# Kernel optimization log

Hardware: AMD Instinct MI355X
Metric: run time of the kernel (lower is better)

## Reference

```python
import jax, jax.numpy as jnp
import numpy as np

B, SEG, MEM, D, E, H = 4, 1024, 1024, 128, 128, 8  # model_dim == embed_dim required by module
TOTAL = SEG + MEM


def sinusoid_pos(length, e):
    # Transformer-XL relative sinusoid table, then flipped so row 0 = largest distance
    p = jnp.arange(length, dtype=jnp.float32)[:, None]
    j = jnp.arange(e, dtype=jnp.float32)[None, :]
    ang = p / jnp.power(jnp.float32(10000.0), 2.0 * j / e)
    enc = jnp.where((jnp.arange(e) % 2 == 0)[None, :], jnp.sin(ang), jnp.cos(ang))
    return enc[::-1]


def circulant_shift(b, shift):
    # b: (B, H, S, W). Row i of the index matrix is the rolled arange shifted by (shift - i).
    W = b.shape[-1]
    S = b.shape[-2]
    idx = jnp.roll(jnp.arange(W), shift)[::-1]
    idx2 = jnp.concatenate([idx, idx])
    win = idx2[jnp.arange(S)[:, None] + jnp.arange(W)[None, :]][:, ::-1]  # (S, W)
    return jnp.take_along_axis(b, win[None, None, :, :], axis=3)


def setup_inputs() -> dict:
    key = jax.random.key(0)
    ks = jax.random.split(key, 11)
    w = 0.02  # small init for linear weights (Linear default-ish scale)
    return {
        "x": jax.random.normal(ks[0], (B, SEG, D), dtype=jnp.float32),
        "mem": jax.random.normal(ks[1], (B, MEM, D), dtype=jnp.float32),
        "att_mask": jnp.zeros((SEG, TOTAL), dtype=bool),  # unused by the module's forward
        "u1": jax.random.normal(ks[2], (H, 1, E), dtype=jnp.float32),
        "u2": jax.random.normal(ks[3], (H, 1, E), dtype=jnp.float32),
        "w_q": jax.random.normal(ks[4], (D, H * E), dtype=jnp.float32) * w,
        "w_kv": jax.random.normal(ks[5], (D, 2 * H * E), dtype=jnp.float32) * w,
        "w_r": jax.random.normal(ks[6], (D, H * E), dtype=jnp.float32) * w,
        "w_mlp": jax.random.normal(ks[7], (H * E, D), dtype=jnp.float32) * w,
        "ln_g": jnp.ones((D,), dtype=jnp.float32),
        "ln_b": jnp.zeros((D,), dtype=jnp.float32),
    }


def reference(x, mem, att_mask, u1, u2, w_q, w_kv, w_r, w_mlp, ln_g, ln_b):
    bsz, seg, d = x.shape
    h = jnp.concatenate((mem, x), axis=1)          # (B, total, D)
    total = h.shape[1]
    mem_len = total - seg

    # NB: the original uses .view without transpose -> plain row-major reshape
    q = (x @ w_q).reshape(bsz, -1, seg, d)          # (B, H, S, E)
    kv = (h @ w_kv).reshape(2 * bsz, -1, total, d)  # (2B, H, T, E)
    k, v = kv[:bsz], kv[bsz:]

    pos = sinusoid_pos(total, d)                    # buffer pos[-total:]
    r = (pos @ w_r).reshape(-1, total, d)           # (H, T, E)

    b = jnp.einsum('bhse,hte->bhst', q, r)
    b = circulant_shift(b, -seg + 1)

    qk = jnp.einsum('bhse,bhte->bhst', q, k)
    u1k = jnp.einsum('he,bhte->bht', u1[:, 0], k)[:, :, None, :]
    u2r = jnp.einsum('he,hte->ht', u2[:, 0], r)[None, :, None, :]

    score = qk + b + u1k + u2r                      # (B, H, S, T)
    tri = (jnp.arange(total)[None, :] - jnp.arange(seg)[:, None]) <= mem_len
    score = jnp.where(tri[None, None], score, 0.0) / jnp.sqrt(jnp.float32(d))
    score = jnp.where(score == 0.0, -jnp.inf, score)  # faithful zeros->-inf trick
    score = jax.nn.softmax(score, axis=-1)

    att = jnp.einsum('bhst,bhte->bhse', score, v).reshape(bsz, seg, -1)
    y = att @ w_mlp + x
    mu = jnp.mean(y, axis=-1, keepdims=True)
    var = jnp.mean((y - mu) ** 2, axis=-1, keepdims=True)
    return (y - mu) / jnp.sqrt(var + 1e-5) * ln_g + ln_b
```

## Files before the change

kernel.cpp:

```cpp
#include <hip/hip_runtime.h>
#include <hip/hip_bf16.h>
#include <stdint.h>

typedef __bf16 bf16;
typedef __attribute__((ext_vector_type(8))) __bf16 bf16x8;
typedef __attribute__((ext_vector_type(4))) __bf16 bf16x4;
typedef __attribute__((ext_vector_type(4))) float f32x4;

#define KSC 0.12764932952880681f

__device__ __forceinline__ f32x4 MFMA(bf16x8 a, bf16x8 b, f32x4 c) {
  return __builtin_amdgcn_mfma_f32_16x16x32_bf16(a, b, c, 0, 0, 0);
}

__device__ __forceinline__ void GLL16(const void* g, void* l) {
  __builtin_amdgcn_global_load_lds(
      (const __attribute__((address_space(1))) void*)g,
      (__attribute__((address_space(3))) void*)l, 16, 0, 0);
}

__device__ __forceinline__ bf16 tobf(float f) { return (bf16)f; }

__global__ __launch_bounds__(256) void k_prep(
    const float* __restrict__ x, const float* __restrict__ mm,
    const float* __restrict__ wq, const float* __restrict__ wkv,
    const float* __restrict__ wr, const float* __restrict__ wmlp,
    bf16* __restrict__ posb, bf16* __restrict__ wq_bt, bf16* __restrict__ wkv_bt,
    bf16* __restrict__ wr_bt, bf16* __restrict__ wmlp_bt,
    bf16* __restrict__ xb, bf16* __restrict__ memb)
{
  __shared__ float T[32][33];
  const int b = blockIdx.x;
  const int tid = threadIdx.x;
  if (b < 1024) {
    int id = b * 256 + tid;
    int t = id >> 7, j = id & 127;
    float p = (float)(2047 - t);
    float ang = p * exp2f(-(float)j * 0.20762050593046264f);
    float v = ((j & 1) == 0) ? __sinf(ang) : __cosf(ang);
    posb[id] = tobf(v);
    return;
  }
  if (b < 1664) {
    int tb = b - 1024;
    const float* src; bf16* dst; int R, C, r0, c0;
    if (tb < 128)      { src = wq;   dst = wq_bt;   R = 128;  C = 1024; r0 = (tb >> 5) * 32;        c0 = (tb & 31) * 32; }
    else if (tb < 384) { int t2 = tb - 128; src = wkv;  dst = wkv_bt;  R = 128;  C = 2048; r0 = (t2 >> 6) * 32; c0 = (t2 & 63) * 32; }
    else if (tb < 512) { int t2 = tb - 384; src = wr;   dst = wr_bt;   R = 128;  C = 1024; r0 = (t2 >> 5) * 32; c0 = (t2 & 31) * 32; }
    else               { int t2 = tb - 512; src = wmlp; dst = wmlp_bt; R = 1024; C = 128;  r0 = (t2 >> 2) * 32; c0 = (t2 & 3) * 32; }
    int r = tid >> 3, c4 = (tid & 7) * 4;
    f32x4 v = *(const f32x4*)(src + (size_t)(r0 + r) * C + c0 + c4);
    T[r][c4] = v[0]; T[r][c4 + 1] = v[1]; T[r][c4 + 2] = v[2]; T[r][c4 + 3] = v[3];
    __syncthreads();
    bf16x4 o;
#pragma unroll
    for (int k = 0; k < 4; ++k) o[k] = tobf(T[c4 + k][r]);
    *(bf16x4*)(dst + (size_t)(c0 + r) * R + r0 + c4) = o;
    return;
  }
  {
    int cb = b - 1664;
    if (cb < 512) {
      int i = cb * 256 + tid;
      f32x4 v = *(const f32x4*)(x + (size_t)i * 4);
      bf16x4 o; o[0]=tobf(v[0]); o[1]=tobf(v[1]); o[2]=tobf(v[2]); o[3]=tobf(v[3]);
      *(bf16x4*)(xb + (size_t)i * 4) = o;
    } else {
      int i = (cb - 512) * 256 + tid;
      f32x4 v = *(const f32x4*)(mm + (size_t)i * 4);
      bf16x4 o; o[0]=tobf(v[0]); o[1]=tobf(v[1]); o[2]=tobf(v[2]); o[3]=tobf(v[3]);
      *(bf16x4*)(memb + (size_t)i * 4) = o;
    }
  }
}

template <int MODE>
__global__ __launch_bounds__(256, 2) void k_proj(
    const bf16* __restrict__ asrc, const bf16* __restrict__ asrc2,
    const bf16* __restrict__ wbt, bf16* __restrict__ out0, bf16* __restrict__ out1,
    const float* __restrict__ u1, const float* __restrict__ u2)
{
  __shared__ bf16 As[64 * 128];
  __shared__ bf16 Bs[128 * 128];
  const int m0 = blockIdx.x * 64;
  const int n0 = blockIdx.y * 128;
  const int tid = threadIdx.x;
  const int w = tid >> 6, lane = tid & 63, g = lane >> 4, c = lane & 15;

#pragma unroll
  for (int it = 0; it < 4; ++it) {
    int ch = w * 256 + it * 64 + lane;
    int row = ch >> 4, cc = ch & 15;
    int scc = cc ^ (row & 7);
    const bf16* src;
    if (MODE == 1) {
      int rg = m0 + row;
      int bb = rg >> 11, t = rg & 2047;
      src = (t < 1024) ? (asrc2 + (size_t)(bb * 1024 + t) * 128)
                       : (asrc + (size_t)(bb * 1024 + (t - 1024)) * 128);
    } else {
      src = asrc + (size_t)(m0 + row) * 128;
    }
    GLL16(src + scc * 8, (char*)As + (w * 256 + it * 64) * 16);
  }
#pragma unroll
  for (int it = 0; it < 8; ++it) {
    int ch = w * 512 + it * 64 + lane;
    int n = ch >> 4, cc = ch & 15;
    int scc = cc ^ (n & 7);
    GLL16(wbt + (size_t)(n0 + n) * 128 + scc * 8, (char*)Bs + (w * 512 + it * 64) * 16);
  }
  __syncthreads();

  f32x4 acc[8] = {};
#pragma unroll
  for (int kk = 0; kk < 4; ++kk) {
    bf16x8 a = *(const bf16x8*)((const char*)As + (16 * w + c) * 256 + (((4 * kk + g) ^ (c & 7)) << 4));
#pragma unroll
    for (int fo = 0; fo < 8; ++fo) {
      bf16x8 b = *(const bf16x8*)((const char*)Bs + (16 * fo + c) * 256 + (((4 * kk + g) ^ (c & 7)) << 4));
      acc[fo] = MFMA(a, b, acc[fo]);
    }
  }

#pragma unroll
  for (int fo = 0; fo < 8; ++fo) {
#pragma unroll
    for (int j = 0; j < 4; ++j) {
      int rg = m0 + 16 * w + 4 * g + j;
      int cg = n0 + 16 * fo + c;
      float av = acc[fo][j];
      if (MODE == 0) {
        int b = rg >> 10, s2 = rg & 1023;
        int nn = s2 >> 7;
        int s = ((s2 & 127) << 3) | (cg >> 7);
        int e = cg & 127;
        size_t idx = ((size_t)((b * 8 + nn) * 1024 + s)) * 128 + e;
        out0[idx] = tobf((av + u1[nn * 128 + e]) * KSC);
        out1[idx] = tobf((av + u2[nn * 128 + e]) * KSC);
      } else if (MODE == 1) {
        int bb = rg >> 11, t = rg & 2047;
        int nn = (t >> 7) & 7;
        int hlf = (t >> 10) & 1;
        int t2 = ((t & 127) << 4) | (cg >> 7);
        int e = cg & 127;
        bf16 v = tobf(av);
        if (bb < 2)
          out0[((size_t)(((2 * bb + hlf) * 8 + nn) * 2048 + t2)) * 128 + e] = v;
        else
          out1[((size_t)(((2 * (bb - 2) + hlf) * 8 + nn) * 2048 + t2)) * 128 + e] = v;
      } else {
        int nn = rg >> 8;
        int t = ((rg & 255) << 3) | (cg >> 7);
        int e = cg & 127;
        bf16 v = tobf(av);
        out0[((size_t)(nn * 2112 + t)) * 128 + e] = v;
        if (t < 64) out0[((size_t)(nn * 2112 + 2048 + t)) * 128 + e] = v;
      }
    }
  }
}

__global__ __launch_bounds__(256) void k_vtrans(const bf16* __restrict__ vh, bf16* __restrict__ vht)
{
  __shared__ bf16 T[64][72];
  int bt = blockIdx.x * 64, be = blockIdx.y * 64, bh = blockIdx.z;
  const bf16* src = vh + (size_t)bh * 2048 * 128;
  bf16* dst = vht + (size_t)bh * 128 * 2048;
#pragma unroll
  for (int i2 = 0; i2 < 2; ++i2) {
    int ch = i2 * 256 + threadIdx.x;
    int tt = ch >> 3, cc = ch & 7;
    bf16x8 v = *(const bf16x8*)(src + (size_t)(bt + tt) * 128 + be + cc * 8);
    *(bf16x8*)&T[tt][cc * 8] = v;
  }
  __syncthreads();
#pragma unroll
  for (int i2 = 0; i2 < 2; ++i2) {
    int ch = i2 * 256 + threadIdx.x;
    int ee = ch >> 3, c2 = ch & 7;
    bf16x8 o;
#pragma unroll
    for (int m = 0; m < 8; ++m) o[m] = T[c2 * 8 + m][ee];
    *(bf16x8*)(dst + (size_t)(be + ee) * 2048 + bt + c2 * 8) = o;
  }
}

__global__ __launch_bounds__(256, 2) void k_flash(
    const bf16* __restrict__ qhk, const bf16* __restrict__ qhr,
    const bf16* __restrict__ kh, const bf16* __restrict__ vht,
    const bf16* __restrict__ rhe, bf16* __restrict__ att2)
{
  __shared__ bf16 Ks[2][64 * 128];
  __shared__ bf16 Vs[2][64 * 128];
  __shared__ char QRS[4][2688];

  const int x = blockIdx.x;
  const int xcd = x & 7;
  const int k2 = x >> 3;
  const int bh = 8 * (k2 & 3) + xcd;
  const int qb = (k2 < 32) ? (k2 >> 2) : (23 - (k2 >> 2));
  const int ib = bh >> 3, nh = bh & 7;
  const int s0 = qb * 64;
  const int tid = threadIdx.x;
  const int w = tid >> 6, lane = tid & 63, g = lane >> 4, c = lane & 15;

  const bf16* qkb  = qhk + (size_t)bh * 1024 * 128;
  const bf16* qrb  = qhr + (size_t)bh * 1024 * 128;
  const bf16* kbase = kh + (size_t)bh * 2048 * 128;
  const bf16* vbase = vht + (size_t)bh * 128 * 2048;
  const bf16* rbase = rhe + (size_t)nh * 2112 * 128;

  const int nt = qb + 17;

  const bf16 *kp0, *kp1, *vp0, *vp1, *vp2, *vp3;
  {
    int ch0 = w * 256 + lane;
    int ch1 = ch0 + 64;
    int r0 = ch0 >> 4, cc0 = ch0 & 15;
    int r1 = ch1 >> 4, cc1 = ch1 & 15;
    kp0 = kbase + (size_t)r0 * 128 + (cc0 ^ (r0 & 7)) * 8;
    kp1 = kbase + (size_t)r1 * 128 + (cc1 ^ (r1 & 7)) * 8;
    int e0 = ch0 >> 3, t0c = ch0 & 7;
    int e1 = ch1 >> 3, t1c = ch1 & 7;
    int e2 = e0 + 16, e3 = e1 + 16;
    vp0 = vbase + (size_t)e0 * 2048 + (t0c ^ (e0 & 7)) * 8;
    vp1 = vbase + (size_t)e1 * 2048 + (t1c ^ (e1 & 7)) * 8;
    vp2 = vbase + (size_t)e2 * 2048 + (t0c ^ (e2 & 7)) * 8;
    vp3 = vbase + (size_t)e3 * 2048 + (t1c ^ (e3 & 7)) * 8;
  }
  const int dof = (w * 256 + lane) * 16;

  auto stage = [&](int pb) {
    char* Kd = (char*)Ks[pb];
    char* Vd = (char*)Vs[pb];
    GLL16(kp0, Kd + dof);
    GLL16(kp1, Kd + dof + 1024);
    GLL16(kp0 + 1024, Kd + dof + 2048);
    GLL16(kp1 + 1024, Kd + dof + 3072);
    GLL16(vp0, Vd + dof);
    GLL16(vp1, Vd + dof + 1024);
    GLL16(vp2, Vd + dof + 2048);
    GLL16(vp3, Vd + dof + 3072);
    kp0 += 8192; kp1 += 8192;
    vp0 += 64; vp1 += 64; vp2 += 64; vp3 += 64;
  };

  bf16x8 qfK[4], qfR[4];
  {
    int srow = s0 + 16 * w + c;
#pragma unroll
    for (int kk = 0; kk < 4; ++kk) {
      qfK[kk] = *(const bf16x8*)(qkb + (size_t)srow * 128 + kk * 32 + g * 8);
      qfR[kk] = *(const bf16x8*)(qrb + (size_t)srow * 128 + kk * 32 + g * 8);
    }
  }

  bf16x8 rf[5][4];
  const bf16* rp[5];
  {
    const int L0 = 1008 - s0 - 16 * w + c;
#pragma unroll
    for (int f2 = 0; f2 < 5; ++f2) {
      rp[f2] = rbase + (size_t)(L0 + 16 * f2) * 128 + g * 8;
#pragma unroll
      for (int kk = 0; kk < 4; ++kk) rf[f2][kk] = *(const bf16x8*)(rp[f2] + kk * 32);
      rp[f2] += 64 * 128;
    }
  }

  f32x4 Ot[8] = {};
  float m_r = -1e30f, l_r = 0.f;

  stage(0);

  for (int tt = 0; tt < nt; ++tt) {
    __syncthreads();
    const bool notlast = (tt + 1 < nt);
    if (notlast) stage((tt + 1) & 1);

    const bf16* Kc = Ks[tt & 1];
    const bf16* Vc = Vs[tt & 1];

    f32x4 sacc[4] = {};
    __builtin_amdgcn_s_setprio(1);
#pragma unroll
    for (int kk = 0; kk < 4; ++kk) {
#pragma unroll
      for (int f = 0; f < 4; ++f) {
        bf16x8 kf = *(const bf16x8*)((const char*)Kc + (16 * f + c) * 256 + (((4 * kk + g) ^ (c & 7)) << 4));
        sacc[f] = MFMA(kf, qfK[kk], sacc[f]);
      }
    }
    f32x4 bacc[5] = {};
#pragma unroll
    for (int f2 = 0; f2 < 5; ++f2)
#pragma unroll
      for (int kk = 0; kk < 4; ++kk)
        bacc[f2] = MFMA(rf[f2][kk], qfR[kk], bacc[f2]);
    __builtin_amdgcn_s_setprio(0);

    bf16* qrw = (bf16*)QRS[w];
#pragma unroll
    for (int f2 = 0; f2 < 5; ++f2)
#pragma unroll
      for (int j = 0; j < 4; ++j)
        qrw[c * 82 + 16 * f2 + 4 * g + j] = tobf(bacc[f2][j]);

    if (notlast) {
#pragma unroll
      for (int f2 = 0; f2 < 5; ++f2) {
#pragma unroll
        for (int kk = 0; kk < 4; ++kk) rf[f2][kk] = *(const bf16x8*)(rp[f2] + kk * 32);
        rp[f2] += 64 * 128;
      }
    }

    float zv[4][4];
#pragma unroll
    for (int f = 0; f < 4; ++f)
#pragma unroll
      for (int j = 0; j < 4; ++j) {
        int tl = 16 * f + 4 * g + j;
        float z = sacc[f][j] + (float)qrw[c * 82 + (tl - c + 15)];
        if (!notlast && (tl > 16 * w + c)) z = -1e30f;
        zv[f][j] = z;
      }

    float pm = fmaxf(fmaxf(fmaxf(zv[0][0], zv[0][1]), fmaxf(zv[0][2], zv[0][3])),
                     fmaxf(fmaxf(zv[1][0], zv[1][1]), fmaxf(zv[1][2], zv[1][3])));
    float pm2 = fmaxf(fmaxf(fmaxf(zv[2][0], zv[2][1]), fmaxf(zv[2][2], zv[2][3])),
                      fmaxf(fmaxf(zv[3][0], zv[3][1]), fmaxf(zv[3][2], zv[3][3])));
    pm = fmaxf(pm, pm2);
    pm = fmaxf(pm, __shfl_xor(pm, 16));
    pm = fmaxf(pm, __shfl_xor(pm, 32));

    float alpha = 1.f;
    if (!__all(pm <= m_r + 8.0f)) {
      float mn = fmaxf(m_r, pm);
      alpha = exp2f(m_r - mn);
      m_r = mn;
      float at[4];
#pragma unroll
      for (int j = 0; j < 4; ++j) at[j] = __shfl(alpha, 20 * g + j);
#pragma unroll
      for (int fo = 0; fo < 8; ++fo)
#pragma unroll
        for (int j = 0; j < 4; ++j) Ot[fo][j] *= at[j];
    }

    float ps = 0.f;
#pragma unroll
    for (int f = 0; f < 4; ++f)
#pragma unroll
      for (int j = 0; j < 4; ++j) { float pp = exp2f(zv[f][j] - m_r); zv[f][j] = pp; ps += pp; }
    ps += __shfl_xor(ps, 16);
    ps += __shfl_xor(ps, 32);
    l_r = l_r * alpha + ps;

    bf16* pw = (bf16*)QRS[w];
#pragma unroll
    for (int f = 0; f < 4; ++f)
#pragma unroll
      for (int j = 0; j < 4; ++j) {
        int t = 16 * f + 4 * g + j;
        pw[c * 80 + ((((t >> 3) ^ (c & 7)) << 3) | (t & 7))] = tobf(zv[f][j]);
      }

    __builtin_amdgcn_s_setprio(1);
#pragma unroll
    for (int kk2 = 0; kk2 < 2; ++kk2) {
      bf16x8 pa = *(const bf16x8*)(pw + c * 80 + (((4 * kk2 + g) ^ (c & 7)) << 3));
#pragma unroll
      for (int fo = 0; fo < 8; ++fo) {
        int e = 16 * fo + c;
        bf16x8 vf = *(const bf16x8*)((const char*)Vc + e * 128 + (((4 * kk2 + g) ^ (c & 7)) << 4));
        Ot[fo] = MFMA(pa, vf, Ot[fo]);
      }
    }
    __builtin_amdgcn_s_setprio(0);
  }

  float linv[4];
#pragma unroll
  for (int j = 0; j < 4; ++j) linv[j] = 1.f / __shfl(l_r, 20 * g + j);
  bf16* ob = att2 + (size_t)ib * 1024 * 1024;
#pragma unroll
  for (int j = 0; j < 4; ++j) {
    int sg = s0 + 16 * w + 4 * g + j;
    size_t rowb = (size_t)(nh * 128 + (sg >> 3)) * 1024 + ((sg & 7) << 7);
#pragma unroll
    for (int fo = 0; fo < 8; ++fo)
      ob[rowb + 16 * fo + c] = tobf(Ot[fo][j] * linv[j]);
  }
}

__global__ __launch_bounds__(256, 2) void k_mlp(
    const bf16* __restrict__ att2, const bf16* __restrict__ wmlp_bt,
    const float* __restrict__ x, const float* __restrict__ lng, const float* __restrict__ lnb,
    float* __restrict__ out)
{
  __shared__ bf16 As[64 * 128];
  __shared__ bf16 Bs[128 * 128];
  const int m0 = blockIdx.x * 64;
  const int tid = threadIdx.x;
  const int w = tid >> 6, lane = tid & 63, g = lane >> 4, c = lane & 15;

  f32x4 acc[8] = {};
  for (int ks = 0; ks < 8; ++ks) {
    int k0 = ks * 128;
    __syncthreads();
#pragma unroll
    for (int it = 0; it < 4; ++it) {
      int ch = w * 256 + it * 64 + lane;
      int row = ch >> 4, cc = ch & 15;
      GLL16(att2 + (size_t)(m0 + row) * 1024 + k0 + ((cc ^ (row & 7)) * 8),
            (char*)As + (w * 256 + it * 64) * 16);
    }
#pragma unroll
    for (int it = 0; it < 8; ++it) {
      int ch = w * 512 + it * 64 + lane;
      int n = ch >> 4, cc = ch & 15;
      GLL16(wmlp_bt + (size_t)n * 1024 + k0 + ((cc ^ (n & 7)) * 8),
            (char*)Bs + (w * 512 + it * 64) * 16);
    }
    __syncthreads();
#pragma unroll
    for (int kk = 0; kk < 4; ++kk) {
      bf16x8 a = *(const bf16x8*)((const char*)As + (16 * w + c) * 256 + (((4 * kk + g) ^ (c & 7)) << 4));
#pragma unroll
      for (int fo = 0; fo < 8; ++fo) {
        bf16x8 b = *(const bf16x8*)((const char*)Bs + (16 * fo + c) * 256 + (((4 * kk + g) ^ (c & 7)) << 4));
        acc[fo] = MFMA(a, b, acc[fo]);
      }
    }
  }
#pragma unroll
  for (int j = 0; j < 4; ++j) {
    int rg = m0 + 16 * w + 4 * g + j;
    float y[8];
    float s1 = 0.f, s2 = 0.f;
#pragma unroll
    for (int fo = 0; fo < 8; ++fo) {
      float v = acc[fo][j] + x[(size_t)rg * 128 + 16 * fo + c];
      y[fo] = v; s1 += v; s2 += v * v;
    }
#pragma unroll
    for (int d = 1; d < 16; d <<= 1) { s1 += __shfl_xor(s1, d); s2 += __shfl_xor(s2, d); }
    float mu = s1 * 0.0078125f;
    float var = s2 * 0.0078125f - mu * mu;
    float rs = rsqrtf(var + 1e-5f);
#pragma unroll
    for (int fo = 0; fo < 8; ++fo) {
      int e = 16 * fo + c;
      out[(size_t)rg * 128 + e] = (y[fo] - mu) * rs * lng[e] + lnb[e];
    }
  }
}

extern "C" void kernel_launch(void* const* d_in, const int* in_sizes, int n_in,
                              void* d_out, int out_size, void* d_ws, size_t ws_size,
                              hipStream_t stream)
{
  const float* x    = (const float*)d_in[0];
  const float* mm   = (const float*)d_in[1];
  const float* u1   = (const float*)d_in[3];
  const float* u2   = (const float*)d_in[4];
  const float* wq   = (const float*)d_in[5];
  const float* wkv  = (const float*)d_in[6];
  const float* wr   = (const float*)d_in[7];
  const float* wmlp = (const float*)d_in[8];
  const float* lng  = (const float*)d_in[9];
  const float* lnb  = (const float*)d_in[10];
  float* out = (float*)d_out;

  char* p = (char*)d_ws;
  bf16* posb    = (bf16*)p;  p += (size_t)262144 * 2;
  bf16* wq_bt   = (bf16*)p;  p += (size_t)131072 * 2;
  bf16* wkv_bt  = (bf16*)p;  p += (size_t)262144 * 2;
  bf16* wr_bt   = (bf16*)p;  p += (size_t)131072 * 2;
  bf16* wmlp_bt = (bf16*)p;  p += (size_t)131072 * 2;
  bf16* xb      = (bf16*)p;  p += (size_t)524288 * 2;
  bf16* memb    = (bf16*)p;  p += (size_t)524288 * 2;
  bf16* qhk     = (bf16*)p;  p += (size_t)4 * 8 * 1024 * 128 * 2;
  bf16* qhr     = (bf16*)p;  p += (size_t)4 * 8 * 1024 * 128 * 2;
  bf16* kh      = (bf16*)p;  p += (size_t)4 * 8 * 2048 * 128 * 2;
  bf16* vh      = (bf16*)p;  p += (size_t)4 * 8 * 2048 * 128 * 2;
  bf16* vht     = (bf16*)p;  p += (size_t)4 * 8 * 2048 * 128 * 2;
  bf16* rhe     = (bf16*)p;  p += (size_t)8 * 2112 * 128 * 2;
  bf16* att2    = (bf16*)p;  p += (size_t)4 * 1024 * 1024 * 2;

  k_prep<<<dim3(2688), dim3(256), 0, stream>>>(x, mm, wq, wkv, wr, wmlp,
                                               posb, wq_bt, wkv_bt, wr_bt, wmlp_bt, xb, memb);
  k_proj<0><<<dim3(64, 8),   dim3(256), 0, stream>>>(xb,  (const bf16*)nullptr, wq_bt,  qhk, qhr, u1, u2);
  k_proj<1><<<dim3(128, 16), dim3(256), 0, stream>>>(xb,  memb,                 wkv_bt, kh,  vh,  nullptr, nullptr);
  k_proj<2><<<dim3(32, 8),   dim3(256), 0, stream>>>(posb,(const bf16*)nullptr, wr_bt,  rhe, (bf16*)nullptr, nullptr, nullptr);
  k_vtrans<<<dim3(32, 2, 32), dim3(256), 0, stream>>>(vh, vht);
  k_flash<<<dim3(512), dim3(256), 0, stream>>>(qhk, qhr, kh, vht, rhe, att2);
  k_mlp<<<dim3(64), dim3(256), 0, stream>>>(att2, wmlp_bt, x, lng, lnb, out);
}
```

Measured before the change: 269.9 us.

## Fuse V transpose into KV projection, vectorize LDS stores, double-buffer MLP

The KV projection now writes V directly in transposed (bh, e, t) layout, which removes the separate transpose kernel and its intermediate buffer. The stores are scattered 2-byte writes with a 4KB stride, so they may coalesce poorly. In the flash kernel the per-lane score and probability writes to LDS are packed into 4-element vector stores, and the bias scratch row stride changes to 84. The MLP kernel double-buffers its LDS tiles so the next K-slice loads while the current one computes, at the cost of more LDS and one block per CU.

After: 304.1 us. 12.6% more time.

```diff
diff --git a/kernel.cpp b/kernel.cpp
--- a/kernel.cpp
+++ b/kernel.cpp
@@ -147,8 +147,10 @@
         bf16 v = tobf(av);
         if (bb < 2)
           out0[((size_t)(((2 * bb + hlf) * 8 + nn) * 2048 + t2)) * 128 + e] = v;
-        else
-          out1[((size_t)(((2 * (bb - 2) + hlf) * 8 + nn) * 2048 + t2)) * 128 + e] = v;
+        else {
+          int bh2 = (2 * (bb - 2) + hlf) * 8 + nn;
+          out1[((size_t)bh2 * 128 + e) * 2048 + t2] = v;
+        }
       } else {
         int nn = rg >> 8;
         int t = ((rg & 255) << 3) | (cg >> 7);
@@ -161,31 +163,6 @@
   }
 }
 
-__global__ __launch_bounds__(256) void k_vtrans(const bf16* __restrict__ vh, bf16* __restrict__ vht)
-{
-  __shared__ bf16 T[64][72];
-  int bt = blockIdx.x * 64, be = blockIdx.y * 64, bh = blockIdx.z;
-  const bf16* src = vh + (size_t)bh * 2048 * 128;
-  bf16* dst = vht + (size_t)bh * 128 * 2048;
-#pragma unroll
-  for (int i2 = 0; i2 < 2; ++i2) {
-    int ch = i2 * 256 + threadIdx.x;
-    int tt = ch >> 3, cc = ch & 7;
-    bf16x8 v = *(const bf16x8*)(src + (size_t)(bt + tt) * 128 + be + cc * 8);
-    *(bf16x8*)&T[tt][cc * 8] = v;
-  }
-  __syncthreads();
-#pragma unroll
-  for (int i2 = 0; i2 < 2; ++i2) {
-    int ch = i2 * 256 + threadIdx.x;
-    int ee = ch >> 3, c2 = ch & 7;
-    bf16x8 o;
-#pragma unroll
-    for (int m = 0; m < 8; ++m) o[m] = T[c2 * 8 + m][ee];
-    *(bf16x8*)(dst + (size_t)(be + ee) * 2048 + bt + c2 * 8) = o;
-  }
-}
-
 __global__ __launch_bounds__(256, 2) void k_flash(
     const bf16* __restrict__ qhk, const bf16* __restrict__ qhr,
     const bf16* __restrict__ kh, const bf16* __restrict__ vht,
@@ -193,7 +170,7 @@
 {
   __shared__ bf16 Ks[2][64 * 128];
   __shared__ bf16 Vs[2][64 * 128];
-  __shared__ char QRS[4][2688];
+  __shared__ bf16 QRS[4][1344];
 
   const int x = blockIdx.x;
   const int xcd = x & 7;
@@ -300,12 +277,14 @@
         bacc[f2] = MFMA(rf[f2][kk], qfR[kk], bacc[f2]);
     __builtin_amdgcn_s_setprio(0);
 
-    bf16* qrw = (bf16*)QRS[w];
-#pragma unroll
-    for (int f2 = 0; f2 < 5; ++f2)
-#pragma unroll
-      for (int j = 0; j < 4; ++j)
-        qrw[c * 82 + 16 * f2 + 4 * g + j] = tobf(bacc[f2][j]);
+    bf16* qrw = &QRS[w][0];
+#pragma unroll
+    for (int f2 = 0; f2 < 5; ++f2) {
+      bf16x4 pk;
+#pragma unroll
+      for (int j = 0; j < 4; ++j) pk[j] = tobf(bacc[f2][j]);
+      *(bf16x4*)(qrw + c * 84 + 16 * f2 + 4 * g) = pk;
+    }
 
     if (notlast) {
 #pragma unroll
@@ -322,7 +301,7 @@
 #pragma unroll
       for (int j = 0; j < 4; ++j) {
         int tl = 16 * f + 4 * g + j;
-        float z = sacc[f][j] + (float)qrw[c * 82 + (tl - c + 15)];
+        float z = sacc[f][j] + (float)qrw[c * 84 + (tl - c + 15)];
         if (!notlast && (tl > 16 * w + c)) z = -1e30f;
         zv[f][j] = z;
       }
@@ -358,14 +337,14 @@
     ps += __shfl_xor(ps, 32);
     l_r = l_r * alpha + ps;
 
-    bf16* pw = (bf16*)QRS[w];
-#pragma unroll
-    for (int f = 0; f < 4; ++f)
-#pragma unroll
-      for (int j = 0; j < 4; ++j) {
-        int t = 16 * f + 4 * g + j;
-        pw[c * 80 + ((((t >> 3) ^ (c & 7)) << 3) | (t & 7))] = tobf(zv[f][j]);
-      }
+    bf16* pw = &QRS[w][0];
+#pragma unroll
+    for (int f = 0; f < 4; ++f) {
+      bf16x4 pk;
+#pragma unroll
+      for (int j = 0; j < 4; ++j) pk[j] = tobf(zv[f][j]);
+      *(bf16x4*)(pw + c * 80 + ((((2 * f + (g >> 1)) ^ (c & 7)) << 3) | (4 * g & 7))) = pk;
+    }
 
     __builtin_amdgcn_s_setprio(1);
 #pragma unroll
@@ -395,42 +374,48 @@
   }
 }
 
-__global__ __launch_bounds__(256, 2) void k_mlp(
+__global__ __launch_bounds__(256, 1) void k_mlp(
     const bf16* __restrict__ att2, const bf16* __restrict__ wmlp_bt,
     const float* __restrict__ x, const float* __restrict__ lng, const float* __restrict__ lnb,
     float* __restrict__ out)
 {
-  __shared__ bf16 As[64 * 128];
-  __shared__ bf16 Bs[128 * 128];
+  __shared__ bf16 As[2][64 * 128];
+  __shared__ bf16 Bs[2][128 * 128];
   const int m0 = blockIdx.x * 64;
   const int tid = threadIdx.x;
   const int w = tid >> 6, lane = tid & 63, g = lane >> 4, c = lane & 15;
 
-  f32x4 acc[8] = {};
-  for (int ks = 0; ks < 8; ++ks) {
+  auto stage = [&](int ks, int pb) {
     int k0 = ks * 128;
-    __syncthreads();
 #pragma unroll
     for (int it = 0; it < 4; ++it) {
       int ch = w * 256 + it * 64 + lane;
       int row = ch >> 4, cc = ch & 15;
       GLL16(att2 + (size_t)(m0 + row) * 1024 + k0 + ((cc ^ (row & 7)) * 8),
-            (char*)As + (w * 256 + it * 64) * 16);
+            (char*)As[pb] + (w * 256 + it * 64) * 16);
     }
 #pragma unroll
     for (int it = 0; it < 8; ++it) {
       int ch = w * 512 + it * 64 + lane;
       int n = ch >> 4, cc = ch & 15;
       GLL16(wmlp_bt + (size_t)n * 1024 + k0 + ((cc ^ (n & 7)) * 8),
-            (char*)Bs + (w * 512 + it * 64) * 16);
-    }
+            (char*)Bs[pb] + (w * 512 + it * 64) * 16);
+    }
+  };
+
+  f32x4 acc[8] = {};
+  stage(0, 0);
+  for (int ks = 0; ks < 8; ++ks) {
     __syncthreads();
+    if (ks + 1 < 8) stage(ks + 1, (ks + 1) & 1);
+    const char* Ac = (const char*)As[ks & 1];
+    const char* Bc = (const char*)Bs[ks & 1];
 #pragma unroll
     for (int kk = 0; kk < 4; ++kk) {
-      bf16x8 a = *(const bf16x8*)((const char*)As + (16 * w + c) * 256 + (((4 * kk + g) ^ (c & 7)) << 4));
+      bf16x8 a = *(const bf16x8*)(Ac + (16 * w + c) * 256 + (((4 * kk + g) ^ (c & 7)) << 4));
 #pragma unroll
       for (int fo = 0; fo < 8; ++fo) {
-        bf16x8 b = *(const bf16x8*)((const char*)Bs + (16 * fo + c) * 256 + (((4 * kk + g) ^ (c & 7)) << 4));
+        bf16x8 b = *(const bf16x8*)(Bc + (16 * fo + c) * 256 + (((4 * kk + g) ^ (c & 7)) << 4));
         acc[fo] = MFMA(a, b, acc[fo]);
       }
     }
@@ -485,7 +470,6 @@
   bf16* qhk     = (bf16*)p;  p += (size_t)4 * 8 * 1024 * 128 * 2;
   bf16* qhr     = (bf16*)p;  p += (size_t)4 * 8 * 1024 * 128 * 2;
   bf16* kh      = (bf16*)p;  p += (size_t)4 * 8 * 2048 * 128 * 2;
-  bf16* vh      = (bf16*)p;  p += (size_t)4 * 8 * 2048 * 128 * 2;
   bf16* vht     = (bf16*)p;  p += (size_t)4 * 8 * 2048 * 128 * 2;
   bf16* rhe     = (bf16*)p;  p += (size_t)8 * 2112 * 128 * 2;
   bf16* att2    = (bf16*)p;  p += (size_t)4 * 1024 * 1024 * 2;
@@ -493,9 +477,8 @@
   k_prep<<<dim3(2688), dim3(256), 0, stream>>>(x, mm, wq, wkv, wr, wmlp,
                                                posb, wq_bt, wkv_bt, wr_bt, wmlp_bt, xb, memb);
   k_proj<0><<<dim3(64, 8),   dim3(256), 0, stream>>>(xb,  (const bf16*)nullptr, wq_bt,  qhk, qhr, u1, u2);
-  k_proj<1><<<dim3(128, 16), dim3(256), 0, stream>>>(xb,  memb,                 wkv_bt, kh,  vh,  nullptr, nullptr);
+  k_proj<1><<<dim3(128, 16), dim3(256), 0, stream>>>(xb,  memb,                 wkv_bt, kh,  vht, nullptr, nullptr);
   k_proj<2><<<dim3(32, 8),   dim3(256), 0, stream>>>(posb,(const bf16*)nullptr, wr_bt,  rhe, (bf16*)nullptr, nullptr, nullptr);
-  k_vtrans<<<dim3(32, 2, 32), dim3(256), 0, stream>>>(vh, vht);
   k_flash<<<dim3(512), dim3(256), 0, stream>>>(qhk, qhr, kh, vht, rhe, att2);
   k_mlp<<<dim3(64), dim3(256), 0, stream>>>(att2, wmlp_bt, x, lng, lnb, out);
 }
```
